# Optimization experiments

Hardware: AMD Instinct MI355X
Metric: run time of the kernel (lower is better)

## Reference

```python
import jax, jax.numpy as jnp
import numpy as np

N_NODES = 50000
N_EDGES = 800000
D_IN = 128
D_OUT = 128


def _gcn_conv(x, W, b, src, dst, num_nodes):
    """PyG GCNConv: h = x @ W^T; symmetric-normalized mean over neighbors
    (with self-loops); out = aggregate + bias.
    src/dst already include self-loops."""
    h = x @ W.T  # [N, C_out]
    ones = jnp.ones(dst.shape[0], dtype=x.dtype)
    deg = jax.ops.segment_sum(ones, dst, num_segments=num_nodes)  # in-degree incl self-loop
    deg_inv_sqrt = jnp.where(deg > 0, jax.lax.rsqrt(deg), 0.0)
    norm = deg_inv_sqrt[src] * deg_inv_sqrt[dst]  # [E+N]
    msgs = h[src] * norm[:, None]  # gather + scale
    out = jax.ops.segment_sum(msgs, dst, num_segments=num_nodes)  # scatter-add
    return out + b


def setup_inputs() -> dict:
    key = jax.random.key(0)
    ks = jax.random.split(key, 9)
    x_r1 = jax.random.normal(ks[0], (N_NODES, D_IN), dtype=jnp.float32)
    x_r2 = jax.random.normal(ks[1], (N_NODES, D_IN), dtype=jnp.float32)
    x_i1 = jax.random.normal(ks[2], (N_NODES, D_IN), dtype=jnp.float32)
    x_i2 = jax.random.normal(ks[3], (N_NODES, D_IN), dtype=jnp.float32)
    edge_index = jax.random.randint(ks[4], (2, N_EDGES), 0, N_NODES, dtype=jnp.int64)
    s = 1.0 / np.sqrt(D_IN)
    W1 = jax.random.uniform(ks[5], (D_OUT, D_IN), minval=-s, maxval=s, dtype=jnp.float32)
    W2 = jax.random.uniform(ks[6], (D_OUT, D_IN), minval=-s, maxval=s, dtype=jnp.float32)
    b1 = jax.random.uniform(ks[7], (D_OUT,), minval=-s, maxval=s, dtype=jnp.float32)
    b2 = jax.random.uniform(ks[8], (D_OUT,), minval=-s, maxval=s, dtype=jnp.float32)
    return {"x_r1": x_r1, "x_r2": x_r2, "x_i1": x_i1, "x_i2": x_i2,
            "edge_index": edge_index, "W1": W1, "b1": b1, "W2": W2, "b2": b2}


def reference(x_r1, x_r2, x_i1, x_i2, edge_index, W1, b1, W2, b2):
    num_nodes = x_r1.shape[0]
    loops = jnp.arange(num_nodes, dtype=edge_index.dtype)
    src = jnp.concatenate([edge_index[0], loops])  # add self-loops
    dst = jnp.concatenate([edge_index[1], loops])
    # real1/imag1 share (W1, b1); real2/imag2 share (W2, b2)
    h_r1 = _gcn_conv(x_r1, W1, b1, src, dst, num_nodes)
    h_r2 = _gcn_conv(x_r2, W2, b2, src, dst, num_nodes)
    h_i1 = _gcn_conv(x_i1, W1, b1, src, dst, num_nodes)
    h_i2 = _gcn_conv(x_i2, W2, b2, src, dst, num_nodes)
    return (h_r1, h_r2, h_i1, h_i2)
```

## Files before the change

### kernel.cpp

```cpp
#include <hip/hip_runtime.h>

#define DD 128

typedef __bf16 bf16x8 __attribute__((ext_vector_type(8)));
typedef float f32x4 __attribute__((ext_vector_type(4)));

static __device__ __forceinline__ unsigned short f2bf(float f) {
    unsigned int u = __float_as_uint(f);
    u += 0x7FFF + ((u >> 16) & 1);
    return (unsigned short)(u >> 16);
}


__global__ void k_zero(int* __restrict__ p, int n) {
    int i = blockIdx.x * 256 + threadIdx.x;
    if (i < n) p[i] = 0;
}

__global__ void k_count(const int* __restrict__ dst, int* __restrict__ cnt, int E) {
    int e = blockIdx.x * 256 + threadIdx.x;
    if (e < E) atomicAdd(&cnt[dst[e]], 1);
}

__global__ __launch_bounds__(1024) void k_scan1(const int* __restrict__ cnt,
                                                int* __restrict__ rp,
                                                float* __restrict__ dinv,
                                                int* __restrict__ bsum,
                                                const float* __restrict__ W1,
                                                const float* __restrict__ W2,
                                                unsigned short* __restrict__ wbf,
                                                int N, int nscan) {
    const int bid = blockIdx.x;
    if (bid >= nscan) {
        int i = (bid - nscan) * 1024 + threadIdx.x;
        float4 v = (i < 4096) ? ((const float4*)W1)[i] : ((const float4*)W2)[i - 4096];
        ushort4 b;
        b.x = f2bf(v.x); b.y = f2bf(v.y); b.z = f2bf(v.z); b.w = f2bf(v.w);
        *(ushort4*)&wbf[(size_t)i * 4] = b;
        return;
    }
    __shared__ int wsum[16];
    const int tid = threadIdx.x, lane = tid & 63, wid = tid >> 6;
    const int i = bid * 1024 + tid;
    int v = (i < N) ? cnt[i] : 0;
    int s = v;
    for (int off = 1; off < 64; off <<= 1) {
        int t = __shfl_up(s, off, 64);
        if (lane >= off) s += t;
    }
    if (lane == 63) wsum[wid] = s;
    __syncthreads();
    int woff = 0, total = 0;
#pragma unroll
    for (int w2 = 0; w2 < 16; ++w2) {
        int t = wsum[w2];
        if (w2 < wid) woff += t;
        total += t;
    }
    if (i < N) {
        rp[i + 1] = woff + s;
        dinv[i] = rsqrtf((float)(v + 1));
    }
    if (tid == 0) bsum[bid] = total;
}

__global__ __launch_bounds__(1024) void k_scan2(const int* __restrict__ bsum,
                                                int* __restrict__ rp, int N) {
    __shared__ int boff_s;
    const int tid = threadIdx.x;
    if (tid < 64) {
        int v = (tid < (int)blockIdx.x) ? bsum[tid] : 0;
        for (int off = 32; off > 0; off >>= 1) v += __shfl_down(v, off, 64);
        if (tid == 0) boff_s = v;
    }
    __syncthreads();
    const int i = blockIdx.x * 1024 + tid;
    if (i < N) rp[i + 1] += boff_s;
    if (i == 0) rp[0] = 0;
}

__global__ void k_fill(const int* __restrict__ ei, const int* __restrict__ rp,
                       int* __restrict__ cnt, const float* __restrict__ dinv,
                       int2* __restrict__ csr, int E) {
    int e = blockIdx.x * 256 + threadIdx.x;
    if (e >= E) return;
    int s = ei[e], d = ei[E + e];
    int old = atomicSub(&cnt[d], 1);
    csr[rp[d] + old - 1] = make_int2(s, __float_as_int(dinv[s]));
}


__global__ __launch_bounds__(512) void k_gemm(
    const float* __restrict__ x0, const float* __restrict__ x1,
    const float* __restrict__ x2, const float* __restrict__ x3,
    const unsigned short* __restrict__ wbf,
    unsigned short* __restrict__ h, int N)
{
    const int m = blockIdx.y;
    const float* x = (m == 0) ? x0 : (m == 1) ? x1 : (m == 2) ? x2 : x3;
    const unsigned short* Wg = wbf + (size_t)(m & 1) * 128 * 128;

    __shared__ unsigned short Ws[128 * 128];
    __shared__ unsigned short ts[128 * 136];

    const int tid = threadIdx.x;
    const int n0 = blockIdx.x * 128;

#pragma unroll
    for (int t = tid; t < 2048; t += 512)
        ((uint4*)Ws)[t] = ((const uint4*)Wg)[t];
    for (int t = tid; t < 128 * 32; t += 512) {
        int r = t >> 5;
        int n = n0 + r;
        float4 v = make_float4(0.f, 0.f, 0.f, 0.f);
        if (n < N) v = ((const float4*)(x + (size_t)n * DD))[t & 31];
        ushort4 b;
        b.x = f2bf(v.x); b.y = f2bf(v.y); b.z = f2bf(v.z); b.w = f2bf(v.w);
        *(ushort4*)&ts[r * 128 + (t & 31) * 4] = b;
    }
    __syncthreads();

    const int w    = tid >> 6;
    const int lane = tid & 63;
    const int am   = lane & 15;
    const int aq   = lane >> 4;
    const int r0   = w * 16;

    f32x4 acc[8] = {};
#pragma unroll
    for (int kk = 0; kk < 128; kk += 32) {
        bf16x8 af = *(const bf16x8*)&ts[(r0 + am) * 128 + kk + aq * 8];
#pragma unroll
        for (int ct = 0; ct < 8; ++ct) {
            bf16x8 bf = *(const bf16x8*)&Ws[(ct * 16 + am) * 128 + kk + aq * 8];
            acc[ct] = __builtin_amdgcn_mfma_f32_16x16x32_bf16(af, bf, acc[ct], 0, 0, 0);
        }
    }
    __syncthreads();

    const int cc = lane & 15;
    const int rr = (lane >> 4) * 4;
#pragma unroll
    for (int ct = 0; ct < 8; ++ct)
#pragma unroll
        for (int i = 0; i < 4; ++i)
            ts[(r0 + rr + i) * 136 + ct * 16 + cc] = f2bf(acc[ct][i]);
    __syncthreads();

#pragma unroll
    for (int k = 0; k < 4; ++k) {
        int f = k * 512 + tid;
        int row = f >> 4, ch = f & 15;
        int n = n0 + row;
        if (n < N) {
            uint4 v = *(const uint4*)&ts[row * 136 + ch * 8];
            *(uint4*)(h + ((size_t)n * 4 + m) * DD + ch * 8) = v;
        }
    }
}


static __device__ __forceinline__ void acc8(float* a, uint4 v, float wt) {
    a[0] += __uint_as_float(v.x << 16) * wt;
    a[1] += __uint_as_float(v.x & 0xffff0000u) * wt;
    a[2] += __uint_as_float(v.y << 16) * wt;
    a[3] += __uint_as_float(v.y & 0xffff0000u) * wt;
    a[4] += __uint_as_float(v.z << 16) * wt;
    a[5] += __uint_as_float(v.z & 0xffff0000u) * wt;
    a[6] += __uint_as_float(v.w << 16) * wt;
    a[7] += __uint_as_float(v.w & 0xffff0000u) * wt;
}

__global__ __launch_bounds__(256) void k_gather(
    const int* __restrict__ rp, const int2* __restrict__ csr,
    const float* __restrict__ dinv, const unsigned short* __restrict__ h,
    const float* __restrict__ b1, const float* __restrict__ b2,
    float* __restrict__ out, int N)
{
    const int n    = blockIdx.x;
    const int tid  = threadIdx.x;
    const int w    = tid >> 6;
    const int lane = tid & 63;
    const int m    = lane >> 4;
    const int c    = (lane & 15) * 8;
    const size_t off = (size_t)lane * 8;

    const float dn = dinv[n];
    float a[8] = {};

    if (w == 3) {
        const float sn = dn * dn;
        const float* bb = (m & 1) ? b2 : b1;
        uint4 hv = *(const uint4*)(h + (size_t)n * 512 + off);
        acc8(a, hv, sn);
        float4 bv0 = *(const float4*)(bb + c);
        float4 bv1 = *(const float4*)(bb + c + 4);
        a[0] += bv0.x; a[1] += bv0.y; a[2] += bv0.z; a[3] += bv0.w;
        a[4] += bv1.x; a[5] += bv1.y; a[6] += bv1.z; a[7] += bv1.w;
    }

    const int j0 = rp[n], j1 = rp[n + 1];
    const int q  = (j1 - j0 + 3) >> 2;
    int jb = j0 + w * q;
    int je = jb + q; if (je > j1) je = j1;

    for (; jb + 3 < je; jb += 4) {
        int2 e0 = csr[jb], e1 = csr[jb + 1], e2 = csr[jb + 2], e3 = csr[jb + 3];
        float w0 = __int_as_float(e0.y) * dn, w1 = __int_as_float(e1.y) * dn,
              w2 = __int_as_float(e2.y) * dn, w3 = __int_as_float(e3.y) * dn;
        uint4 v0 = *(const uint4*)(h + (size_t)e0.x * 512 + off);
        uint4 v1 = *(const uint4*)(h + (size_t)e1.x * 512 + off);
        uint4 v2 = *(const uint4*)(h + (size_t)e2.x * 512 + off);
        uint4 v3 = *(const uint4*)(h + (size_t)e3.x * 512 + off);
        acc8(a, v0, w0); acc8(a, v1, w1); acc8(a, v2, w2); acc8(a, v3, w3);
    }
    for (; jb < je; ++jb) {
        int2 e = csr[jb];
        float wt = __int_as_float(e.y) * dn;
        uint4 v = *(const uint4*)(h + (size_t)e.x * 512 + off);
        acc8(a, v, wt);
    }

    __shared__ float part[3][64][8];
    if (w) {
        *(f32x4*)&part[w - 1][lane][0] = *(f32x4*)&a[0];
        *(f32x4*)&part[w - 1][lane][4] = *(f32x4*)&a[4];
    }
    __syncthreads();
    if (w == 0) {
#pragma unroll
        for (int k = 0; k < 3; ++k)
#pragma unroll
            for (int i = 0; i < 8; ++i) a[i] += part[k][lane][i];
        float* po = out + ((size_t)m * N + n) * DD + c;
        f32x4 r0, r1;
        r0.x = a[0]; r0.y = a[1]; r0.z = a[2]; r0.w = a[3];
        r1.x = a[4]; r1.y = a[5]; r1.z = a[6]; r1.w = a[7];
        __builtin_nontemporal_store(r0, (f32x4*)po);
        __builtin_nontemporal_store(r1, (f32x4*)(po + 4));
    }
}


extern "C" void kernel_launch(void* const* d_in, const int* in_sizes, int n_in,
                              void* d_out, int out_size, void* d_ws, size_t ws_size,
                              hipStream_t stream) {
    const float* x0 = (const float*)d_in[0];
    const float* x1 = (const float*)d_in[1];
    const float* x2 = (const float*)d_in[2];
    const float* x3 = (const float*)d_in[3];
    const int*   ei = (const int*)d_in[4];
    const float* W1 = (const float*)d_in[5];
    const float* b1 = (const float*)d_in[6];
    const float* W2 = (const float*)d_in[7];
    const float* b2 = (const float*)d_in[8];
    float* out = (float*)d_out;

    const int N = in_sizes[0] / DD;
    const int E = in_sizes[4] / 2;

    int*   cnt  = (int*)d_ws;
    int*   rp   = cnt + 65536;
    float* dinv = (float*)(rp + 65536);
    int*   bsum = (int*)(dinv + 65536);
    unsigned short* wbf = (unsigned short*)(bsum + 256);
    int2*  csr  = (int2*)(wbf + 2 * 128 * 128);
    unsigned short* h = (unsigned short*)(csr + E);

    const int nscan = (N + 1023) / 1024;

    k_zero <<<(N + 255) / 256, 256, 0, stream>>>(cnt, N);
    k_count<<<(E + 255) / 256, 256, 0, stream>>>(ei + E, cnt, E);
    k_scan1<<<nscan + 8, 1024, 0, stream>>>(cnt, rp, dinv, bsum, W1, W2, wbf, N, nscan);
    k_scan2<<<nscan, 1024, 0, stream>>>(bsum, rp, N);
    k_fill <<<(E + 255) / 256, 256, 0, stream>>>(ei, rp, cnt, dinv, csr, E);

    dim3 g((N + 127) / 128, 4);
    k_gemm<<<g, 512, 0, stream>>>(x0, x1, x2, x3, wbf, h, N);

    k_gather<<<N, 256, 0, stream>>>(rp, csr, dinv, h, b1, b2, out, N);
}
```

Baseline: 427.6 us.

## Map one wavefront per node in gather, swizzle GEMM LDS, vectorize CSR build

The gather kernel now gives each 64-lane wavefront its own node instead of splitting one node's edges across four wavefronts. This removes the shared-memory reduction and the block barrier, and cuts the block count by four, but each node's edges are now processed serially by one wave. The GEMM LDS tiles get an XOR swizzle to reduce bank conflicts on the MFMA operand reads. The count and fill kernels process 4 and 2 edges per thread with vector index loads, and the zeroing kernel is replaced by hipMemsetAsync. The vectorized count and fill assume E is divisible by 4 and 2.

```diff
diff --git a/kernel.cpp b/kernel.cpp
--- a/kernel.cpp
+++ b/kernel.cpp
@@ -12,14 +12,13 @@
 }
 
 
-__global__ void k_zero(int* __restrict__ p, int n) {
-    int i = blockIdx.x * 256 + threadIdx.x;
-    if (i < n) p[i] = 0;
-}
-
 __global__ void k_count(const int* __restrict__ dst, int* __restrict__ cnt, int E) {
-    int e = blockIdx.x * 256 + threadIdx.x;
-    if (e < E) atomicAdd(&cnt[dst[e]], 1);
+    int e4 = (blockIdx.x * 256 + threadIdx.x) * 4;
+    if (e4 < E) {
+        int4 d = *(const int4*)&dst[e4];
+        atomicAdd(&cnt[d.x], 1); atomicAdd(&cnt[d.y], 1);
+        atomicAdd(&cnt[d.z], 1); atomicAdd(&cnt[d.w], 1);
+    }
 }
 
 __global__ __launch_bounds__(1024) void k_scan1(const int* __restrict__ cnt,
@@ -82,11 +81,14 @@
 __global__ void k_fill(const int* __restrict__ ei, const int* __restrict__ rp,
                        int* __restrict__ cnt, const float* __restrict__ dinv,
                        int2* __restrict__ csr, int E) {
-    int e = blockIdx.x * 256 + threadIdx.x;
-    if (e >= E) return;
-    int s = ei[e], d = ei[E + e];
-    int old = atomicSub(&cnt[d], 1);
-    csr[rp[d] + old - 1] = make_int2(s, __float_as_int(dinv[s]));
+    int e2 = (blockIdx.x * 256 + threadIdx.x) * 2;
+    if (e2 >= E) return;
+    int2 s = *(const int2*)&ei[e2];
+    int2 d = *(const int2*)&ei[E + e2];
+    int o0 = atomicSub(&cnt[d.x], 1);
+    csr[rp[d.x] + o0 - 1] = make_int2(s.x, __float_as_int(dinv[s.x]));
+    int o1 = atomicSub(&cnt[d.y], 1);
+    csr[rp[d.y] + o1 - 1] = make_int2(s.y, __float_as_int(dinv[s.y]));
 }
 
 
@@ -108,7 +110,7 @@
 
 #pragma unroll
     for (int t = tid; t < 2048; t += 512)
-        ((uint4*)Ws)[t] = ((const uint4*)Wg)[t];
+        ((uint4*)Ws)[t ^ ((t >> 4) & 7)] = ((const uint4*)Wg)[t];
     for (int t = tid; t < 128 * 32; t += 512) {
         int r = t >> 5;
         int n = n0 + r;
@@ -116,7 +118,7 @@
         if (n < N) v = ((const float4*)(x + (size_t)n * DD))[t & 31];
         ushort4 b;
         b.x = f2bf(v.x); b.y = f2bf(v.y); b.z = f2bf(v.z); b.w = f2bf(v.w);
-        *(ushort4*)&ts[r * 128 + (t & 31) * 4] = b;
+        *(ushort4*)&ts[r * 128 + (((t & 31) * 4) ^ ((r & 7) << 3))] = b;
     }
     __syncthreads();
 
@@ -129,10 +131,12 @@
     f32x4 acc[8] = {};
 #pragma unroll
     for (int kk = 0; kk < 128; kk += 32) {
-        bf16x8 af = *(const bf16x8*)&ts[(r0 + am) * 128 + kk + aq * 8];
+        const int ar = r0 + am;
+        bf16x8 af = *(const bf16x8*)&ts[ar * 128 + ((kk + aq * 8) ^ ((ar & 7) << 3))];
 #pragma unroll
         for (int ct = 0; ct < 8; ++ct) {
-            bf16x8 bf = *(const bf16x8*)&Ws[(ct * 16 + am) * 128 + kk + aq * 8];
+            bf16x8 bf = *(const bf16x8*)&Ws[(ct * 16 + am) * 128 +
+                                            ((kk + aq * 8) ^ ((am & 7) << 3))];
             acc[ct] = __builtin_amdgcn_mfma_f32_16x16x32_bf16(af, bf, acc[ct], 0, 0, 0);
         }
     }
@@ -177,34 +181,31 @@
     const float* __restrict__ b1, const float* __restrict__ b2,
     float* __restrict__ out, int N)
 {
-    const int n    = blockIdx.x;
-    const int tid  = threadIdx.x;
-    const int w    = tid >> 6;
-    const int lane = tid & 63;
+    const int n = blockIdx.x * 4 + (threadIdx.x >> 6);
+    if (n >= N) return;
+    const int lane = threadIdx.x & 63;
     const int m    = lane >> 4;
     const int c    = (lane & 15) * 8;
     const size_t off = (size_t)lane * 8;
 
     const float dn = dinv[n];
-    float a[8] = {};
-
-    if (w == 3) {
+    float a[8];
+
+    {
         const float sn = dn * dn;
         const float* bb = (m & 1) ? b2 : b1;
         uint4 hv = *(const uint4*)(h + (size_t)n * 512 + off);
-        acc8(a, hv, sn);
         float4 bv0 = *(const float4*)(bb + c);
         float4 bv1 = *(const float4*)(bb + c + 4);
-        a[0] += bv0.x; a[1] += bv0.y; a[2] += bv0.z; a[3] += bv0.w;
-        a[4] += bv1.x; a[5] += bv1.y; a[6] += bv1.z; a[7] += bv1.w;
-    }
-
-    const int j0 = rp[n], j1 = rp[n + 1];
-    const int q  = (j1 - j0 + 3) >> 2;
-    int jb = j0 + w * q;
-    int je = jb + q; if (je > j1) je = j1;
-
-    for (; jb + 3 < je; jb += 4) {
+        a[0] = bv0.x; a[1] = bv0.y; a[2] = bv0.z; a[3] = bv0.w;
+        a[4] = bv1.x; a[5] = bv1.y; a[6] = bv1.z; a[7] = bv1.w;
+        acc8(a, hv, sn);
+    }
+
+    int jb = rp[n];
+    const int j1 = rp[n + 1];
+
+    for (; jb + 3 < j1; jb += 4) {
         int2 e0 = csr[jb], e1 = csr[jb + 1], e2 = csr[jb + 2], e3 = csr[jb + 3];
         float w0 = __int_as_float(e0.y) * dn, w1 = __int_as_float(e1.y) * dn,
               w2 = __int_as_float(e2.y) * dn, w3 = __int_as_float(e3.y) * dn;
@@ -214,31 +215,19 @@
         uint4 v3 = *(const uint4*)(h + (size_t)e3.x * 512 + off);
         acc8(a, v0, w0); acc8(a, v1, w1); acc8(a, v2, w2); acc8(a, v3, w3);
     }
-    for (; jb < je; ++jb) {
+    for (; jb < j1; ++jb) {
         int2 e = csr[jb];
         float wt = __int_as_float(e.y) * dn;
         uint4 v = *(const uint4*)(h + (size_t)e.x * 512 + off);
         acc8(a, v, wt);
     }
 
-    __shared__ float part[3][64][8];
-    if (w) {
-        *(f32x4*)&part[w - 1][lane][0] = *(f32x4*)&a[0];
-        *(f32x4*)&part[w - 1][lane][4] = *(f32x4*)&a[4];
-    }
-    __syncthreads();
-    if (w == 0) {
-#pragma unroll
-        for (int k = 0; k < 3; ++k)
-#pragma unroll
-            for (int i = 0; i < 8; ++i) a[i] += part[k][lane][i];
-        float* po = out + ((size_t)m * N + n) * DD + c;
-        f32x4 r0, r1;
-        r0.x = a[0]; r0.y = a[1]; r0.z = a[2]; r0.w = a[3];
-        r1.x = a[4]; r1.y = a[5]; r1.z = a[6]; r1.w = a[7];
-        __builtin_nontemporal_store(r0, (f32x4*)po);
-        __builtin_nontemporal_store(r1, (f32x4*)(po + 4));
-    }
+    float* po = out + ((size_t)m * N + n) * DD + c;
+    f32x4 r0, r1;
+    r0.x = a[0]; r0.y = a[1]; r0.z = a[2]; r0.w = a[3];
+    r1.x = a[4]; r1.y = a[5]; r1.z = a[6]; r1.w = a[7];
+    __builtin_nontemporal_store(r0, (f32x4*)po);
+    __builtin_nontemporal_store(r1, (f32x4*)(po + 4));
 }
 
 
@@ -269,14 +258,14 @@
 
     const int nscan = (N + 1023) / 1024;
 
-    k_zero <<<(N + 255) / 256, 256, 0, stream>>>(cnt, N);
-    k_count<<<(E + 255) / 256, 256, 0, stream>>>(ei + E, cnt, E);
+    hipMemsetAsync(cnt, 0, (size_t)N * sizeof(int), stream);
+    k_count<<<(E / 4 + 255) / 256, 256, 0, stream>>>(ei + E, cnt, E);
     k_scan1<<<nscan + 8, 1024, 0, stream>>>(cnt, rp, dinv, bsum, W1, W2, wbf, N, nscan);
     k_scan2<<<nscan, 1024, 0, stream>>>(bsum, rp, N);
-    k_fill <<<(E + 255) / 256, 256, 0, stream>>>(ei, rp, cnt, dinv, csr, E);
+    k_fill <<<(E / 2 + 255) / 256, 256, 0, stream>>>(ei, rp, cnt, dinv, csr, E);
 
     dim3 g((N + 127) / 128, 4);
     k_gemm<<<g, 512, 0, stream>>>(x0, x1, x2, x3, wbf, h, N);
 
-    k_gather<<<N, 256, 0, stream>>>(rp, csr, dinv, h, b1, b2, out, N);
-}
+    k_gather<<<(N + 3) / 4, 256, 0, stream>>>(rp, csr, dinv, h, b1, b2, out, N);
+}
```

New measurement: 418.8 us. 2.1% less time.
